# Kernel tuning notes

Measured on AMD Instinct MI355X. Metric: run time of the kernel, lower is better.

The kernel has to match this reference:

```python
import jax, jax.numpy as jnp
import numpy as np
from jax import lax

TS = 1.0  # sampling time


def setup_inputs() -> dict:
    key = jax.random.key(0)
    k1, k2, k3, k4 = jax.random.split(key, 4)
    q, m, n_x, n_u, h = 8192, 2048, 2, 1, 64
    x0 = jax.random.normal(k1, (q, n_x), dtype=jnp.float32)
    u = jax.random.normal(k2, (m, q, n_u), dtype=jnp.float32)
    # small neural state-space model: f(x, u) = tanh([x, u] @ W1 + b1) @ W2 + b2
    W1 = jax.random.normal(k3, (n_x + n_u, h), dtype=jnp.float32) * (1.0 / np.sqrt(n_x + n_u))
    b1 = jnp.zeros((h,), dtype=jnp.float32)
    W2 = jax.random.normal(k4, (h, n_x), dtype=jnp.float32) * 0.01
    b2 = jnp.zeros((n_x,), dtype=jnp.float32)
    return {"x0": x0, "u": u, "W1": W1, "b1": b1, "W2": W2, "b2": b2}


def reference(x0, u, W1, b1, W2, b2):
    ts = TS
    dt2 = ts / 2.0

    def f(x, u_step):
        # x: (q, n_x), u_step: (q, n_u) -> dx: (q, n_x)
        h = jnp.tanh(jnp.concatenate([x, u_step], axis=-1) @ W1 + b1)
        return h @ W2 + b2

    def step(x, u_step):
        k1 = f(x, u_step)
        k2 = f(x + dt2 * k1, u_step)
        k3 = f(x + dt2 * k2, u_step)
        k4 = f(x + ts * k3, u_step)
        x_new = x + (ts / 6.0) * (k1 + 2.0 * k2 + 2.0 * k3 + k4)
        return x_new, x  # output is state BEFORE update (matches torch loop)

    _, X_sim = lax.scan(step, x0, u)
    return X_sim  # (m, q, n_x)
```

## Files before the change

### kernel.cpp

```cpp
#include <hip/hip_runtime.h>

#define QN 8192
#define MN 2048
#define HN 64
#define LPT 16
#define UPL 4

template <int CTRL>
__device__ __forceinline__ float dpp_add(float v) {
    int m = __builtin_amdgcn_update_dpp(0, __float_as_int(v), CTRL, 0xf, 0xf, true);
    return v + __int_as_float(m);
}
#define DPP_QUAD_XOR1 0xB1
#define DPP_QUAD_XOR2 0x4E
#define DPP_HALF_MIRR 0x141
#define DPP_ROW_MIRR  0x140

__global__ __launch_bounds__(256, 2) void rk4_nss_kernel(
    const float* __restrict__ x0p,
    const float* __restrict__ up,
    const float* __restrict__ W1,
    const float* __restrict__ b1,
    const float* __restrict__ W2,
    const float* __restrict__ b2,
    float* __restrict__ out)
{
    const int tid  = blockIdx.x * 256 + threadIdx.x;
    const int lane = threadIdx.x & (LPT - 1);
    const int traj = tid >> 4;
    if (traj >= QN) return;

    const float SC = 2.8853900817779268f;
    const float CL = 27.0f;

    float ws10[UPL], ws11[UPL], ws12[UPL], bsb[UPL], w20n[UPL], w21n[UPL];
#pragma unroll
    for (int k = 0; k < UPL; ++k) {
        const int j = lane + k * LPT;
        ws10[k] = W1[j] * SC;
        ws11[k] = W1[HN + j] * SC;
        ws12[k] = W1[2 * HN + j] * SC;
        bsb[k]  = b1[j] * SC;
        w20n[k] = -2.0f * W2[2 * j];
        w21n[k] = -2.0f * W2[2 * j + 1];
    }
    float c0 = b2[0], c1 = b2[1];
    for (int j = 0; j < HN; ++j) {
        c0 += W2[2 * j];
        c1 += W2[2 * j + 1];
    }

    float xa = x0p[2 * traj];
    float xb = x0p[2 * traj + 1];
    float ucur = up[traj];

    float2* outv = reinterpret_cast<float2*>(out);

    float pb[UPL];

    auto feval = [&](float ia, float ib, float& d0, float& d1) {
        float den[UPL];
#pragma unroll
        for (int k = 0; k < UPL; ++k) {
            float pre = fmaf(ws10[k], ia, fmaf(ws11[k], ib, pb[k]));
            pre = __builtin_amdgcn_fmed3f(pre, -CL, CL);
            den[k] = __builtin_amdgcn_exp2f(pre) + 1.0f;
        }
        float d01 = den[0] * den[1];
        float d23 = den[2] * den[3];
        float r   = __builtin_amdgcn_rcpf(d01 * d23);
        float r01 = r * d23;
        float r23 = r * d01;
        float inv0 = r01 * den[1];
        float inv1 = r01 * den[0];
        float inv2 = r23 * den[3];
        float inv3 = r23 * den[2];

        float p0 = fmaf(inv0, w20n[0],
                   fmaf(inv1, w20n[1],
                   fmaf(inv2, w20n[2], inv3 * w20n[3])));
        float p1 = fmaf(inv0, w21n[0],
                   fmaf(inv1, w21n[1],
                   fmaf(inv2, w21n[2], inv3 * w21n[3])));

        p0 = dpp_add<DPP_QUAD_XOR1>(p0);  p1 = dpp_add<DPP_QUAD_XOR1>(p1);
        p0 = dpp_add<DPP_QUAD_XOR2>(p0);  p1 = dpp_add<DPP_QUAD_XOR2>(p1);
        p0 = dpp_add<DPP_HALF_MIRR>(p0);  p1 = dpp_add<DPP_HALF_MIRR>(p1);
        p0 = dpp_add<DPP_ROW_MIRR>(p0);   p1 = dpp_add<DPP_ROW_MIRR>(p1);
        d0 = p0 + c0;
        d1 = p1 + c1;
    };

    for (int t = 0; t < MN; ++t) {
        if (lane == 0) {
            outv[t * QN + traj] = make_float2(xa, xb);
        }
        const float unext = (t + 1 < MN) ? up[(t + 1) * QN + traj] : 0.0f;

#pragma unroll
        for (int k = 0; k < UPL; ++k)
            pb[k] = fmaf(ws12[k], ucur, bsb[k]);

        float k1a, k1b, k2a, k2b, k3a, k3b, k4a, k4b;
        feval(xa, xb, k1a, k1b);
        feval(fmaf(0.5f, k1a, xa), fmaf(0.5f, k1b, xb), k2a, k2b);
        feval(fmaf(0.5f, k2a, xa), fmaf(0.5f, k2b, xb), k3a, k3b);
        feval(xa + k3a, xb + k3b, k4a, k4b);

        float ta = k2a + k3a;
        float sa = k1a + k4a;
        xa = fmaf((1.0f / 6.0f), fmaf(2.0f, ta, sa), xa);
        float tb = k2b + k3b;
        float sb = k1b + k4b;
        xb = fmaf((1.0f / 6.0f), fmaf(2.0f, tb, sb), xb);
        ucur = unext;
    }
}

extern "C" void kernel_launch(void* const* d_in, const int* in_sizes, int n_in,
                              void* d_out, int out_size, void* d_ws, size_t ws_size,
                              hipStream_t stream) {
    const float* x0 = (const float*)d_in[0];
    const float* u  = (const float*)d_in[1];
    const float* W1 = (const float*)d_in[2];
    const float* b1 = (const float*)d_in[3];
    const float* W2 = (const float*)d_in[4];
    const float* b2 = (const float*)d_in[5];
    float* out = (float*)d_out;

    const int threads = 256;
    const int blocks  = (QN * LPT) / threads;
    rk4_nss_kernel<<<blocks, threads, 0, stream>>>(x0, u, W1, b1, W2, b2, out);
}
```

Baseline: 1.947 ms.

## Spread each trajectory over 32 lanes using permlane32 swap reduction

Each trajectory now uses 32 lanes instead of 16, so each lane holds two hidden units instead of four. Two trajectories share a wave, with each trajectory's lanes split across the two 32-lane halves. A permlane32_swap step is added to the DPP butterfly to finish the cross-half sum, and launch bounds raise the blocks-per-CU hint from 2 to 4. The aim is to shorten the serial per-step dependency chain by giving each lane less work, at the cost of twice as many threads and one extra cross-lane operation per function evaluation.

```diff
diff --git a/kernel.cpp b/kernel.cpp
--- a/kernel.cpp
+++ b/kernel.cpp
@@ -1,10 +1,12 @@
 #include <hip/hip_runtime.h>
+
+typedef int v2i __attribute__((ext_vector_type(2)));
 
 #define QN 8192
 #define MN 2048
 #define HN 64
-#define LPT 16
-#define UPL 4
+#define LPT 32
+#define UPL 2
 
 template <int CTRL>
 __device__ __forceinline__ float dpp_add(float v) {
@@ -16,7 +18,13 @@
 #define DPP_HALF_MIRR 0x141
 #define DPP_ROW_MIRR  0x140
 
-__global__ __launch_bounds__(256, 2) void rk4_nss_kernel(
+__device__ __forceinline__ float xor32_add(float p) {
+    v2i pr = __builtin_amdgcn_permlane32_swap(__float_as_int(p), __float_as_int(p),
+                                              false, false);
+    return __int_as_float(pr.x) + __int_as_float(pr.y);
+}
+
+__global__ __launch_bounds__(256, 4) void rk4_nss_kernel(
     const float* __restrict__ x0p,
     const float* __restrict__ up,
     const float* __restrict__ W1,
@@ -25,10 +33,12 @@
     const float* __restrict__ b2,
     float* __restrict__ out)
 {
-    const int tid  = blockIdx.x * 256 + threadIdx.x;
-    const int lane = threadIdx.x & (LPT - 1);
-    const int traj = tid >> 4;
-    if (traj >= QN) return;
+    const int tid    = blockIdx.x * 256 + threadIdx.x;
+    const int lane64 = threadIdx.x & 63;
+    const int wid    = tid >> 6;
+    const int group  = (lane64 >> 4) & 1;
+    const int traj   = 2 * wid + group;
+    const int s      = (lane64 & 15) + ((lane64 & 32) >> 1);
 
     const float SC = 2.8853900817779268f;
     const float CL = 27.0f;
@@ -36,7 +46,7 @@
     float ws10[UPL], ws11[UPL], ws12[UPL], bsb[UPL], w20n[UPL], w21n[UPL];
 #pragma unroll
     for (int k = 0; k < UPL; ++k) {
-        const int j = lane + k * LPT;
+        const int j = s + k * 32;
         ws10[k] = W1[j] * SC;
         ws11[k] = W1[HN + j] * SC;
         ws12[k] = W1[2 * HN + j] * SC;
@@ -55,6 +65,7 @@
     float ucur = up[traj];
 
     float2* outv = reinterpret_cast<float2*>(out);
+    const bool writer = ((lane64 & 47) == 0);
 
     float pb[UPL];
 
@@ -67,32 +78,24 @@
             den[k] = __builtin_amdgcn_exp2f(pre) + 1.0f;
         }
         float d01 = den[0] * den[1];
-        float d23 = den[2] * den[3];
-        float r   = __builtin_amdgcn_rcpf(d01 * d23);
-        float r01 = r * d23;
-        float r23 = r * d01;
-        float inv0 = r01 * den[1];
-        float inv1 = r01 * den[0];
-        float inv2 = r23 * den[3];
-        float inv3 = r23 * den[2];
+        float r   = __builtin_amdgcn_rcpf(d01);
+        float inv0 = r * den[1];
+        float inv1 = r * den[0];
 
-        float p0 = fmaf(inv0, w20n[0],
-                   fmaf(inv1, w20n[1],
-                   fmaf(inv2, w20n[2], inv3 * w20n[3])));
-        float p1 = fmaf(inv0, w21n[0],
-                   fmaf(inv1, w21n[1],
-                   fmaf(inv2, w21n[2], inv3 * w21n[3])));
+        float p0 = fmaf(inv0, w20n[0], inv1 * w20n[1]);
+        float p1 = fmaf(inv0, w21n[0], inv1 * w21n[1]);
 
         p0 = dpp_add<DPP_QUAD_XOR1>(p0);  p1 = dpp_add<DPP_QUAD_XOR1>(p1);
         p0 = dpp_add<DPP_QUAD_XOR2>(p0);  p1 = dpp_add<DPP_QUAD_XOR2>(p1);
         p0 = dpp_add<DPP_HALF_MIRR>(p0);  p1 = dpp_add<DPP_HALF_MIRR>(p1);
         p0 = dpp_add<DPP_ROW_MIRR>(p0);   p1 = dpp_add<DPP_ROW_MIRR>(p1);
+        p0 = xor32_add(p0);               p1 = xor32_add(p1);
         d0 = p0 + c0;
         d1 = p1 + c1;
     };
 
     for (int t = 0; t < MN; ++t) {
-        if (lane == 0) {
+        if (writer) {
             outv[t * QN + traj] = make_float2(xa, xb);
         }
         const float unext = (t + 1 < MN) ? up[(t + 1) * QN + traj] : 0.0f;
```

After: 2.502 ms. 1.28x slower.

## Use 8 lanes per trajectory with 8 hidden units per lane

Applied to the files above, without the earlier changes.

Each trajectory is now handled by 8 lanes instead of 16, and each lane processes 8 hidden units instead of 4. This halves the number of threads and drops one DPP reduction stage per function evaluation. The reciprocal trick now pairs units two at a time, which adds reciprocal ops per lane. Launch bounds drop to one block per SM to give each thread more registers, so there is less parallelism to hide the serial RK4 dependency chain.

```diff
diff --git a/kernel.cpp b/kernel.cpp
--- a/kernel.cpp
+++ b/kernel.cpp
@@ -3,8 +3,8 @@
 #define QN 8192
 #define MN 2048
 #define HN 64
-#define LPT 16
-#define UPL 4
+#define LPT 8
+#define UPL 8
 
 template <int CTRL>
 __device__ __forceinline__ float dpp_add(float v) {
@@ -14,9 +14,8 @@
 #define DPP_QUAD_XOR1 0xB1
 #define DPP_QUAD_XOR2 0x4E
 #define DPP_HALF_MIRR 0x141
-#define DPP_ROW_MIRR  0x140
 
-__global__ __launch_bounds__(256, 2) void rk4_nss_kernel(
+__global__ __launch_bounds__(256, 1) void rk4_nss_kernel(
     const float* __restrict__ x0p,
     const float* __restrict__ up,
     const float* __restrict__ W1,
@@ -27,7 +26,7 @@
 {
     const int tid  = blockIdx.x * 256 + threadIdx.x;
     const int lane = threadIdx.x & (LPT - 1);
-    const int traj = tid >> 4;
+    const int traj = tid >> 3;
     if (traj >= QN) return;
 
     const float SC = 2.8853900817779268f;
@@ -55,6 +54,7 @@
     float ucur = up[traj];
 
     float2* outv = reinterpret_cast<float2*>(out);
+    const bool writer = (lane == 0);
 
     float pb[UPL];
 
@@ -66,33 +66,26 @@
             pre = __builtin_amdgcn_fmed3f(pre, -CL, CL);
             den[k] = __builtin_amdgcn_exp2f(pre) + 1.0f;
         }
-        float d01 = den[0] * den[1];
-        float d23 = den[2] * den[3];
-        float r   = __builtin_amdgcn_rcpf(d01 * d23);
-        float r01 = r * d23;
-        float r23 = r * d01;
-        float inv0 = r01 * den[1];
-        float inv1 = r01 * den[0];
-        float inv2 = r23 * den[3];
-        float inv3 = r23 * den[2];
-
-        float p0 = fmaf(inv0, w20n[0],
-                   fmaf(inv1, w20n[1],
-                   fmaf(inv2, w20n[2], inv3 * w20n[3])));
-        float p1 = fmaf(inv0, w21n[0],
-                   fmaf(inv1, w21n[1],
-                   fmaf(inv2, w21n[2], inv3 * w21n[3])));
+        float p0 = 0.0f, p1 = 0.0f;
+#pragma unroll
+        for (int k = 0; k < UPL; k += 2) {
+            float d01 = den[k] * den[k + 1];
+            float r   = __builtin_amdgcn_rcpf(d01);
+            float inv0 = r * den[k + 1];
+            float inv1 = r * den[k];
+            p0 = fmaf(inv0, w20n[k], fmaf(inv1, w20n[k + 1], p0));
+            p1 = fmaf(inv0, w21n[k], fmaf(inv1, w21n[k + 1], p1));
+        }
 
         p0 = dpp_add<DPP_QUAD_XOR1>(p0);  p1 = dpp_add<DPP_QUAD_XOR1>(p1);
         p0 = dpp_add<DPP_QUAD_XOR2>(p0);  p1 = dpp_add<DPP_QUAD_XOR2>(p1);
         p0 = dpp_add<DPP_HALF_MIRR>(p0);  p1 = dpp_add<DPP_HALF_MIRR>(p1);
-        p0 = dpp_add<DPP_ROW_MIRR>(p0);   p1 = dpp_add<DPP_ROW_MIRR>(p1);
         d0 = p0 + c0;
         d1 = p1 + c1;
     };
 
     for (int t = 0; t < MN; ++t) {
-        if (lane == 0) {
+        if (writer) {
             outv[t * QN + traj] = make_float2(xa, xb);
         }
         const float unext = (t + 1 < MN) ? up[(t + 1) * QN + traj] : 0.0f;
```

Result: slower. 2.053 ms (+5.4%).
